# Optimization experiments

Hardware: AMD Instinct MI355X
Metric: run time of the kernel (lower is better)

Reference implementation:

```python
import jax, jax.numpy as jnp
import numpy as np

DIM = 2048
N_HEADS = 16
HEAD_DIM = DIM // N_HEADS
SEQ = 1024
BSZ = 2
ADAPTER_LEN = 10
MAX_FEATS = 10
ROPE_THETA = 10000.0


def setup_inputs() -> dict:
    key = jax.random.key(0)
    ks = jax.random.split(key, 10)
    x = jax.random.normal(ks[0], (BSZ, SEQ, DIM), dtype=jnp.float32)
    adapter = jax.random.normal(ks[1], (1, ADAPTER_LEN, DIM), dtype=jnp.float32)
    # causal additive mask [1,1,S,S]
    neg = jnp.full((SEQ, SEQ), -1e9, dtype=jnp.float32)
    mask = jnp.triu(neg, k=1)[None, None]
    # rotary frequencies (real/imag of freqs_cis)
    inv_freq = 1.0 / (ROPE_THETA ** (np.arange(0, HEAD_DIM, 2, dtype=np.float32) / HEAD_DIM))
    t = np.arange(SEQ, dtype=np.float32)
    ang = jnp.asarray(np.outer(t, inv_freq), dtype=jnp.float32)  # [S, HEAD_DIM//2]
    freqs_cos = jnp.cos(ang)
    freqs_sin = jnp.sin(ang)
    scale = 0.02
    wq = jax.random.normal(ks[2], (DIM, DIM), dtype=jnp.float32) * scale
    wk = jax.random.normal(ks[3], (DIM, DIM), dtype=jnp.float32) * scale
    wv = jax.random.normal(ks[4], (DIM, DIM), dtype=jnp.float32) * scale
    wo = jax.random.normal(ks[5], (DIM, DIM), dtype=jnp.float32) * scale
    gate1 = jax.random.normal(ks[6], (1, N_HEADS, 1, 1), dtype=jnp.float32) * 0.5
    gate2 = jnp.ones((1, N_HEADS, 1, 1), dtype=jnp.float32) * -3.0
    return {"x": x, "adapter": adapter, "mask": mask, "freqs_cos": freqs_cos,
            "freqs_sin": freqs_sin, "wq": wq, "wk": wk, "wv": wv, "wo": wo,
            "gate1": gate1, "gate2": gate2, "video_start": 30}


def _apply_rope(t, cos, sin):
    # t: [B,S,H,D]; cos/sin: [S, D//2] -> complex multiply on consecutive pairs
    tr = t.reshape(*t.shape[:-1], HEAD_DIM // 2, 2)
    xr, xi = tr[..., 0], tr[..., 1]
    c = cos[None, :, None, :]
    s = sin[None, :, None, :]
    out_r = xr * c - xi * s
    out_i = xr * s + xi * c
    return jnp.stack([out_r, out_i], axis=-1).reshape(t.shape)


def reference(x, adapter, mask, freqs_cos, freqs_sin, wq, wk, wv, wo, gate1, gate2, video_start):
    bsz, seqlen, _ = x.shape
    al = adapter.shape[1]
    vs = int(video_start)
    # projections (torch Linear: y = x @ W^T)
    xq = (x @ wq.T).reshape(bsz, seqlen, N_HEADS, HEAD_DIM)
    xk = (x @ wk.T).reshape(bsz, seqlen, N_HEADS, HEAD_DIM)
    xv = (x @ wv.T).reshape(bsz, seqlen, N_HEADS, HEAD_DIM)
    xq = _apply_rope(xq, freqs_cos, freqs_sin)
    xk = _apply_rope(xk, freqs_cos, freqs_sin)
    # adapter keys/values (no RoPE), broadcast over batch
    a_k = (adapter @ wk.T).reshape(1, al, N_HEADS, HEAD_DIM)
    a_v = (adapter @ wv.T).reshape(1, al, N_HEADS, HEAD_DIM)
    a_k = jnp.broadcast_to(a_k, (bsz, al, N_HEADS, HEAD_DIM))
    a_v = jnp.broadcast_to(a_v, (bsz, al, N_HEADS, HEAD_DIM))
    keys = jnp.concatenate([a_k, xk], axis=1)      # [B, al+S, H, D]
    values = jnp.concatenate([a_v, xv], axis=1)
    # mask extended with zeros over adapter columns
    extra = jnp.zeros((1, 1, seqlen, al), dtype=mask.dtype)
    full_mask = jnp.concatenate([extra, mask], axis=-1)
    scores = jnp.einsum('bqhd,bkhd->bhqk', xq, keys) / jnp.sqrt(jnp.float32(HEAD_DIM))
    scores = scores + full_mask
    # split softmax: adapter part gated by tanh(gate1)
    adapter_scores = jax.nn.softmax(scores[..., :al], axis=-1) * jnp.tanh(gate1)
    vt = scores[..., al:]
    vt = vt.at[:, :, vs + MAX_FEATS:, vs:vs + MAX_FEATS].add(gate2)
    vt = jax.nn.softmax(vt, axis=-1)
    probs = jnp.concatenate([adapter_scores, vt], axis=-1)  # [B,H,S,al+S]
    out = jnp.einsum('bhqk,bkhd->bqhd', probs, values)
    out = out.reshape(bsz, seqlen, DIM)
    return out @ wo.T
```

## Files before the change

### kernel.cpp

```cpp
#include <hip/hip_runtime.h>
#include <math.h>

#define DIM   2048
#define NH    16
#define HD    128
#define SEQQ  1024
#define BSZ   2
#define AL    10
#define MAXF  10
#define KVROWS (SEQQ + AL)
#define BK    32
#define VTP   2080

typedef unsigned short ushort_t;
typedef __bf16   bf16x8 __attribute__((ext_vector_type(8)));
typedef float    f32x4  __attribute__((ext_vector_type(4)));
typedef ushort_t us8    __attribute__((ext_vector_type(8)));

#define AS1 __attribute__((address_space(1)))
#define AS3 __attribute__((address_space(3)))

__device__ __forceinline__ float b2f(ushort_t u) {
    return __uint_as_float(((unsigned int)u) << 16);
}
__device__ __forceinline__ ushort_t f2b(float f) {
    unsigned int u = __float_as_uint(f);
    u += 0x7fffu + ((u >> 16) & 1u);
    return (ushort_t)(u >> 16);
}
__device__ __forceinline__ float scrub(float v, float canary) {
    return ((__float_as_uint(v) & 0x7f800000u) == 0x7f800000u) ? canary : v;
}
__device__ __forceinline__ bf16x8 cvt8(const float* p) {
    float4 a = *(const float4*)p;
    float4 b = *(const float4*)(p + 4);
    us8 u;
    u[0] = f2b(a.x); u[1] = f2b(a.y); u[2] = f2b(a.z); u[3] = f2b(a.w);
    u[4] = f2b(b.x); u[5] = f2b(b.y); u[6] = f2b(b.z); u[7] = f2b(b.w);
    return *(bf16x8*)&u;
}

__global__ __launch_bounds__(256) void cvt5(
    const float* __restrict__ s0, const float* __restrict__ s1,
    const float* __restrict__ s2, const float* __restrict__ s3,
    const float* __restrict__ s4,
    ushort_t* __restrict__ d0, ushort_t* __restrict__ d1,
    ushort_t* __restrict__ d2, ushort_t* __restrict__ d3,
    ushort_t* __restrict__ d4)
{
    const int y = blockIdx.y;
    const float* s = (y == 0) ? s0 : (y == 1) ? s1 : (y == 2) ? s2 : (y == 3) ? s3 : s4;
    ushort_t*    d = (y == 0) ? d0 : (y == 1) ? d1 : (y == 2) ? d2 : (y == 3) ? d3 : d4;
    size_t i = (size_t)blockIdx.x * 256 + threadIdx.x;
    float4 a = ((const float4*)s)[2 * i];
    float4 b = ((const float4*)s)[2 * i + 1];
    us8 u;
    u[0] = f2b(a.x); u[1] = f2b(a.y); u[2] = f2b(a.z); u[3] = f2b(a.w);
    u[4] = f2b(b.x); u[5] = f2b(b.y); u[6] = f2b(b.z); u[7] = f2b(b.w);
    *(us8*)(d + i * 8) = u;
}

__global__ __launch_bounds__(256) void adapter_gemm(
    const float* __restrict__ adp,
    const ushort_t* __restrict__ Wkb, const ushort_t* __restrict__ Wvb,
    ushort_t* __restrict__ Ko, ushort_t* __restrict__ VtO,
    float canary)
{
    __shared__ ushort_t Al[AL * DIM];

    const int t = threadIdx.x;
    #pragma unroll
    for (int p = 0; p < 10; ++p) {
        int i = p * 256 + t;
        const float* sp = adp + i * 8;
        float4 a = *(const float4*)sp;
        float4 b = *(const float4*)(sp + 4);
        us8 u;
        u[0] = f2b(a.x); u[1] = f2b(a.y); u[2] = f2b(a.z); u[3] = f2b(a.w);
        u[4] = f2b(b.x); u[5] = f2b(b.y); u[6] = f2b(b.z); u[7] = f2b(b.w);
        *(us8*)(Al + i * 8) = u;
    }
    __syncthreads();

    const int z = blockIdx.x >> 8;
    const ushort_t* W = z ? Wvb : Wkb;
    const int nbase = (blockIdx.x & 255) * 8;
    const int w = t >> 6, lane = t & 63;

    #pragma unroll
    for (int nn = 0; nn < 2; ++nn) {
        const int n = nbase + w * 2 + nn;
        const ushort_t* wr = W + (size_t)n * DIM;
        float acc[AL] = {};
        #pragma unroll
        for (int c = 0; c < 4; ++c) {
            const int k = c * 512 + lane * 8;
            us8 b8 = *(const us8*)(wr + k);
            float bf[8];
            #pragma unroll
            for (int j = 0; j < 8; ++j) bf[j] = b2f(b8[j]);
            #pragma unroll
            for (int m = 0; m < AL; ++m) {
                us8 a8 = *(const us8*)(Al + m * DIM + k);
                #pragma unroll
                for (int j = 0; j < 8; ++j)
                    acc[m] = fmaf(b2f(a8[j]), bf[j], acc[m]);
            }
        }
        #pragma unroll
        for (int m = 0; m < AL; ++m) {
            float v = acc[m];
            v += __shfl_xor(v, 1);  v += __shfl_xor(v, 2);
            v += __shfl_xor(v, 4);  v += __shfl_xor(v, 8);
            v += __shfl_xor(v, 16); v += __shfl_xor(v, 32);
            if (lane == 0) {
                ushort_t ov = f2b(scrub(v, canary));
                if (z) VtO[(size_t)n * VTP + 2048 + m] = ov;
                else   Ko[(size_t)m * DIM + n] = ov;
            }
        }
        if (z && lane < 22) VtO[(size_t)n * VTP + 2058 + lane] = 0;
    }
}

template<int MODE>
__global__ __launch_bounds__(256) void gemm_bt(
    const ushort_t* __restrict__ A,
    const ushort_t* __restrict__ B0, const ushort_t* __restrict__ B1, const ushort_t* __restrict__ B2,
    void* __restrict__ C0, void* __restrict__ C1, void* __restrict__ C2,
    const float* __restrict__ fc, const float* __restrict__ fs,
    float qscale, float canary)
{
    __shared__ ushort_t As[128 * 32];
    __shared__ ushort_t Bs[128 * 32];

    const int lid  = blockIdx.x + (blockIdx.y << 4) + (blockIdx.z << 8);
    const int cpx  = (int)(gridDim.z << 5);
    const int wgid = (lid & 7) * cpx + (lid >> 3);
    const int z    = wgid >> 8;
    const int rem  = wgid & 255;
    const int m0   = (rem >> 4) << 7;
    const int n0   = (rem & 15) << 7;

    const ushort_t* B = (z == 0) ? B0 : (z == 1) ? B1 : B2;
    void*           C = (z == 0) ? C0 : (z == 1) ? C1 : C2;

    const int t = threadIdx.x;
    const int w = t >> 6, lane = t & 63;
    const int ln = lane & 15, qd = lane >> 4;
    const int wrow = (w >> 1) * 64, wcol = (w & 1) * 64;

    const int r0 = t >> 2, c0 = (t & 3) * 8;
    const int r1 = (t + 256) >> 2;
    const ushort_t* Ag0 = A + (size_t)(m0 + r0) * DIM + c0;
    const ushort_t* Ag1 = A + (size_t)(m0 + r1) * DIM + c0;
    const ushort_t* Bg0 = B + (size_t)(n0 + r0) * DIM + c0;
    const ushort_t* Bg1 = B + (size_t)(n0 + r1) * DIM + c0;
    ushort_t* Al0 = As + (size_t)t * 8;
    ushort_t* Al1 = As + (size_t)(t + 256) * 8;
    ushort_t* Bl0 = Bs + (size_t)t * 8;
    ushort_t* Bl1 = Bs + (size_t)(t + 256) * 8;

    f32x4 acc[4][4] = {};

    for (int k0 = 0; k0 < DIM; k0 += BK) {
        if (k0) __syncthreads();
        __builtin_amdgcn_global_load_lds((const AS1 void*)(Ag0 + k0), (AS3 void*)Al0, 16, 0, 0);
        __builtin_amdgcn_global_load_lds((const AS1 void*)(Ag1 + k0), (AS3 void*)Al1, 16, 0, 0);
        __builtin_amdgcn_global_load_lds((const AS1 void*)(Bg0 + k0), (AS3 void*)Bl0, 16, 0, 0);
        __builtin_amdgcn_global_load_lds((const AS1 void*)(Bg1 + k0), (AS3 void*)Bl1, 16, 0, 0);
        __syncthreads();

        bf16x8 af[4], bfr[4];
        #pragma unroll
        for (int i = 0; i < 4; ++i) {
            af[i]  = *(const bf16x8*)(As + (wrow + i * 16 + ln) * 32 + qd * 8);
            bfr[i] = *(const bf16x8*)(Bs + (wcol + i * 16 + ln) * 32 + qd * 8);
        }
        #pragma unroll
        for (int i = 0; i < 4; ++i)
            #pragma unroll
            for (int j = 0; j < 4; ++j)
                acc[i][j] = __builtin_amdgcn_mfma_f32_16x16x32_bf16(af[i], bfr[j], acc[i][j], 0, 0, 0);
    }

    const float rsc = (MODE == 0 && z == 0) ? qscale : 1.0f;

    #pragma unroll
    for (int i = 0; i < 4; ++i) {
        #pragma unroll
        for (int j = 0; j < 4; ++j) {
            const int gn = n0 + wcol + j * 16 + ln;
            const int gm0 = m0 + wrow + i * 16 + qd * 4;
            if (MODE == 0 && z == 2) {
                ushort4 ov;
                ov.x = f2b(scrub(acc[i][j][0], canary));
                ov.y = f2b(scrub(acc[i][j][1], canary));
                ov.z = f2b(scrub(acc[i][j][2], canary));
                ov.w = f2b(scrub(acc[i][j][3], canary));
                *(ushort4*)((ushort_t*)C + (size_t)gn * VTP + gm0) = ov;
            } else if (MODE == 0) {
                const int fidx = (gn & 127) >> 1;
                #pragma unroll
                for (int r = 0; r < 4; ++r) {
                    const int gm = gm0 + r;
                    float v = scrub(acc[i][j][r], canary);
                    float po = __shfl_xor(v, 1);
                    const int fo = ((gm & 1023) << 6) + fidx;
                    float c = fc[fo], s = fs[fo];
                    float ov = (ln & 1) ? (po * s + v * c) : (v * c - po * s);
                    ((ushort_t*)C)[(size_t)gm * DIM + gn] = f2b(ov * rsc);
                }
            } else {
                #pragma unroll
                for (int r = 0; r < 4; ++r) {
                    float v = scrub(acc[i][j][r], canary);
                    ((float*)C)[(size_t)(gm0 + r) * DIM + gn] = v;
                }
            }
        }
    }
}

__global__ __launch_bounds__(256) void gemm_wo(
    const ushort_t* __restrict__ A,
    const ushort_t* __restrict__ W,
    float* __restrict__ C, float canary)
{
    __shared__ ushort_t As[128 * 32];
    __shared__ ushort_t Bs[64 * 32];

    const int lid  = blockIdx.x + (blockIdx.y << 5);
    const int wgid = (lid & 7) * 64 + (lid >> 3);
    const int m0 = (wgid >> 5) << 7;
    const int n0 = (wgid & 31) << 6;

    const int t = threadIdx.x;
    const int w = t >> 6, lane = t & 63;
    const int ln = lane & 15, qd = lane >> 4;
    const int wrow = (w >> 1) * 64, wcol = (w & 1) * 32;

    const int r0 = t >> 2, c0 = (t & 3) * 8;
    const int r1 = (t + 256) >> 2;
    const ushort_t* Ag0 = A + (size_t)(m0 + r0) * DIM + c0;
    const ushort_t* Ag1 = A + (size_t)(m0 + r1) * DIM + c0;
    const ushort_t* Bg0 = W + (size_t)(n0 + r0) * DIM + c0;
    ushort_t* Al0 = As + (size_t)t * 8;
    ushort_t* Al1 = As + (size_t)(t + 256) * 8;
    ushort_t* Bl0 = Bs + (size_t)t * 8;

    f32x4 acc[4][2] = {};

    for (int k0 = 0; k0 < DIM; k0 += BK) {
        if (k0) __syncthreads();
        __builtin_amdgcn_global_load_lds((const AS1 void*)(Ag0 + k0), (AS3 void*)Al0, 16, 0, 0);
        __builtin_amdgcn_global_load_lds((const AS1 void*)(Ag1 + k0), (AS3 void*)Al1, 16, 0, 0);
        __builtin_amdgcn_global_load_lds((const AS1 void*)(Bg0 + k0), (AS3 void*)Bl0, 16, 0, 0);
        __syncthreads();

        bf16x8 af[4], bfr[2];
        #pragma unroll
        for (int i = 0; i < 4; ++i)
            af[i] = *(const bf16x8*)(As + (wrow + i * 16 + ln) * 32 + qd * 8);
        #pragma unroll
        for (int j = 0; j < 2; ++j)
            bfr[j] = *(const bf16x8*)(Bs + (wcol + j * 16 + ln) * 32 + qd * 8);
        #pragma unroll
        for (int i = 0; i < 4; ++i)
            #pragma unroll
            for (int j = 0; j < 2; ++j)
                acc[i][j] = __builtin_amdgcn_mfma_f32_16x16x32_bf16(af[i], bfr[j], acc[i][j], 0, 0, 0);
    }

    #pragma unroll
    for (int i = 0; i < 4; ++i)
        #pragma unroll
        for (int j = 0; j < 2; ++j) {
            const int gn = n0 + wcol + j * 16 + ln;
            const int gm0 = m0 + wrow + i * 16 + qd * 4;
            #pragma unroll
            for (int r = 0; r < 4; ++r)
                C[(size_t)(gm0 + r) * DIM + gn] = scrub(acc[i][j][r], canary);
        }
}

template<bool AF32, bool CF32>
__global__ __launch_bounds__(256) void mfma_gemm(
    const void* __restrict__ Av,
    const float* __restrict__ B0, const float* __restrict__ B1, const float* __restrict__ B2,
    void* __restrict__ C0, void* __restrict__ C1, void* __restrict__ C2,
    int M, float canary)
{
    const int z = blockIdx.z;
    const float* B = (z == 0) ? B0 : (z == 1) ? B1 : B2;
    void*       C = (z == 0) ? C0 : (z == 1) ? C1 : C2;

    const int m0 = blockIdx.y * 128;
    const int n0 = blockIdx.x * 128;
    const int t    = threadIdx.x;
    const int w    = t >> 6;
    const int lane = t & 63;
    const int ln   = lane & 15, qd = lane >> 4;
    const int wrow = (w >> 1) * 64, wcol = (w & 1) * 64;

    size_t aoff[4];
    const float* brow[4];
    #pragma unroll
    for (int i = 0; i < 4; ++i) {
        int gr = m0 + wrow + i * 16 + ln; gr = (gr < M) ? gr : (M - 1);
        aoff[i] = (size_t)gr * DIM + qd * 8;
        brow[i] = B + (size_t)(n0 + wcol + i * 16 + ln) * DIM + qd * 8;
    }

    f32x4 acc[4][4] = {};

    for (int k0 = 0; k0 < DIM; k0 += BK) {
        bf16x8 af[4], bfr[4];
        #pragma unroll
        for (int i = 0; i < 4; ++i) {
            if (AF32) af[i] = cvt8((const float*)Av + aoff[i] + k0);
            else      af[i] = *(const bf16x8*)((const ushort_t*)Av + aoff[i] + k0);
            bfr[i] = cvt8(brow[i] + k0);
        }
        #pragma unroll
        for (int i = 0; i < 4; ++i)
            #pragma unroll
            for (int j = 0; j < 4; ++j)
                acc[i][j] = __builtin_amdgcn_mfma_f32_16x16x32_bf16(af[i], bfr[j], acc[i][j], 0, 0, 0);
    }

    #pragma unroll
    for (int i = 0; i < 4; ++i) {
        #pragma unroll
        for (int j = 0; j < 4; ++j) {
            const int gn = n0 + wcol + j * 16 + ln;
            #pragma unroll
            for (int r = 0; r < 4; ++r) {
                const int gm = m0 + wrow + i * 16 + qd * 4 + r;
                float v = scrub(acc[i][j][r], canary);
                if (gm < M) {
                    if (CF32) ((float*)C)[(size_t)gm * DIM + gn] = v;
                    else      ((ushort_t*)C)[(size_t)gm * DIM + gn] = f2b(v);
                }
            }
        }
    }
}

__global__ __launch_bounds__(256) void rope_kernel(ushort_t* __restrict__ Qb,
                                                   ushort_t* __restrict__ Kb,
                                                   const float* __restrict__ fc,
                                                   const float* __restrict__ fs,
                                                   float qscale)
{
    int i = blockIdx.x * 256 + threadIdx.x;
    ushort_t* T = blockIdx.y ? Kb : Qb;
    const float sc = blockIdx.y ? 1.0f : qscale;
    int row = i >> 10;
    int p   = i & 1023;
    float c = fc[((row & 1023) << 6) + (p & 63)];
    float s = fs[((row & 1023) << 6) + (p & 63)];
    ushort_t* ptr = T + (size_t)row * DIM + p * 2;
    float xr = b2f(ptr[0]), xi = b2f(ptr[1]);
    ptr[0] = f2b((xr * c - xi * s) * sc);
    ptr[1] = f2b((xr * s + xi * c) * sc);
}

__global__ __launch_bounds__(256) void attn_mfma(const ushort_t* __restrict__ Q,
                                                 const ushort_t* __restrict__ Kg,
                                                 const ushort_t* __restrict__ Vt,
                                                 const float* __restrict__ g1,
                                                 const float* __restrict__ g2,
                                                 const int* __restrict__ vsp,
                                                 ushort_t* __restrict__ AO)
{
    __shared__ ushort_t Kls[2][64 * 128];
    __shared__ ushort_t Vls[2][128 * 64];
    __shared__ ushort_t Pl[4 * 16 * 72];

    const int blk = blockIdx.x;
    const int wg   = (blk & 7) * 64 + (blk >> 3);
    const int gidx = wg >> 4;
    const int mem  = wg & 15;
    const int qtb  = (mem & 1) ? (mem >> 1) : (15 - (mem >> 1));
    const int qt   = ((gidx >> 1) & 1) ? (15 - qtb) : qtb;
    const int h = gidx & 15;
    const int b = gidx >> 4;
    const int q0  = qt * 64;
    const int nsteps = qt + 1;
    const int t = threadIdx.x;
    const int w = t >> 6, lane = t & 63;
    const int ln = lane & 15, g = lane >> 4;
    const int hb = h * HD;
    const size_t kvb = (size_t)b << 10;
    const int vs = *vsp;
    const float g2h = g2[h];
    const float ag  = tanhf(g1[h]);
    const int gq = q0 + w * 16 + ln;

    const ushort_t* qrow = Q + (kvb + gq) * DIM + hb;
    bf16x8 qf[4];
    #pragma unroll
    for (int c = 0; c < 4; ++c) qf[c] = *(const bf16x8*)(qrow + g * 8 + 32 * c);

    auto stage = [&](int bi, int k0) {
        #pragma unroll
        for (int p = 0; p < 4; ++p) {
            int i = t + 256 * p;
            int kr = i >> 4, ks = (i & 15) ^ (kr & 7);
            __builtin_amdgcn_global_load_lds(
                (const AS1 void*)(Kg + (kvb + k0 + kr) * DIM + hb + ks * 8),
                (AS3 void*)(&Kls[bi][i * 8]), 16, 0, 0);
        }
        #pragma unroll
        for (int p = 0; p < 4; ++p) {
            int i = t + 256 * p;
            int vr = i >> 3, vsl = (i & 7) ^ (vr & 7);
            __builtin_amdgcn_global_load_lds(
                (const AS1 void*)(Vt + (size_t)(hb + vr) * VTP + kvb + k0 + vsl * 8),
                (AS3 void*)(&Vls[bi][i * 8]), 16, 0, 0);
        }
    };

    stage(0, 0);

    f32x4 oa[8] = {};
    float m_run = -1e30f, l_run = 0.f;
    ushort_t* Plw = Pl + w * (16 * 72) + ln * 72;

    for (int s = 0; s < nsteps; ++s) {
        const int k0 = s * 64;
        const int cur = s & 1;
        __syncthreads();
        if (s + 1 < nsteps) stage(cur ^ 1, k0 + 64);

        f32x4 sc[4] = {};
        __builtin_amdgcn_s_setprio(1);
        #pragma unroll
        for (int mt = 0; mt < 4; ++mt) {
            const int krow = ln + 16 * mt;
            const ushort_t* krp = &Kls[cur][krow * 128];
            #pragma unroll
            for (int c = 0; c < 4; ++c) {
                bf16x8 kf = *(const bf16x8*)(krp + ((8 * g + 32 * c) ^ ((krow & 7) << 3)));
                sc[mt] = __builtin_amdgcn_mfma_f32_16x16x32_bf16(kf, qf[c], sc[mt], 0, 0, 0);
            }
        }
        __builtin_amdgcn_s_setprio(0);

        float mloc = -3e38f;
        #pragma unroll
        for (int mt = 0; mt < 4; ++mt)
            #pragma unroll
            for (int r = 0; r < 4; ++r) {
                int gk = k0 + mt * 16 + g * 4 + r;
                float v = sc[mt][r];
                if (gk > gq) v -= 1e9f;
                if (gk >= vs && gk < vs + MAXF && gq >= vs + MAXF) v += g2h;
                sc[mt][r] = v;
                mloc = fmaxf(mloc, v);
            }
        mloc = fmaxf(mloc, __shfl_xor(mloc, 16));
        mloc = fmaxf(mloc, __shfl_xor(mloc, 32));
        const float m_new = fmaxf(m_run, mloc);
        const float alpha = __expf(m_run - m_new);
        float psum = 0.f;
        #pragma unroll
        for (int mt = 0; mt < 4; ++mt) {
            float p0 = __expf(sc[mt][0] - m_new);
            float p1 = __expf(sc[mt][1] - m_new);
            float p2 = __expf(sc[mt][2] - m_new);
            float p3 = __expf(sc[mt][3] - m_new);
            psum += (p0 + p1) + (p2 + p3);
            uint2 pw_;
            pw_.x = (unsigned)f2b(p0) | ((unsigned)f2b(p1) << 16);
            pw_.y = (unsigned)f2b(p2) | ((unsigned)f2b(p3) << 16);
            *(uint2*)(Plw + mt * 16 + g * 4) = pw_;
        }
        psum += __shfl_xor(psum, 16);
        psum += __shfl_xor(psum, 32);
        l_run = l_run * alpha + psum;
        m_run = m_new;
        #pragma unroll
        for (int i = 0; i < 8; ++i) {
            oa[i][0] *= alpha; oa[i][1] *= alpha; oa[i][2] *= alpha; oa[i][3] *= alpha;
        }

        bf16x8 pf0 = *(const bf16x8*)(Plw + 8 * g);
        bf16x8 pf1 = *(const bf16x8*)(Plw + 32 + 8 * g);
        __builtin_amdgcn_s_setprio(1);
        #pragma unroll
        for (int dt = 0; dt < 8; ++dt) {
            const int vrow = dt * 16 + ln;
            const ushort_t* vrp = &Vls[cur][vrow * 64];
            bf16x8 vf0 = *(const bf16x8*)(vrp + ((g     ^ (vrow & 7)) * 8));
            bf16x8 vf1 = *(const bf16x8*)(vrp + (((g+4) ^ (vrow & 7)) * 8));
            oa[dt] = __builtin_amdgcn_mfma_f32_16x16x32_bf16(vf0, pf0, oa[dt], 0, 0, 0);
            oa[dt] = __builtin_amdgcn_mfma_f32_16x16x32_bf16(vf1, pf1, oa[dt], 0, 0, 0);
        }
        __builtin_amdgcn_s_setprio(0);
    }

    const float invl = 1.f / l_run;
    #pragma unroll
    for (int i = 0; i < 8; ++i) {
        oa[i][0] *= invl; oa[i][1] *= invl; oa[i][2] *= invl; oa[i][3] *= invl;
    }

    const ushort_t* karow = Kg + (size_t)(2048 + (ln < 10 ? ln : 9)) * DIM + hb;
    f32x4 sa4 = {};
    #pragma unroll
    for (int c = 0; c < 4; ++c) {
        bf16x8 kf = *(const bf16x8*)(karow + 8 * g + 32 * c);
        sa4 = __builtin_amdgcn_mfma_f32_16x16x32_bf16(kf, qf[c], sa4, 0, 0, 0);
    }
    float am = -3e38f;
    float pa[4];
    #pragma unroll
    for (int r = 0; r < 4; ++r) {
        int kl = g * 4 + r;
        pa[r] = (kl < 10) ? sa4[r] : -1e30f;
        am = fmaxf(am, pa[r]);
    }
    am = fmaxf(am, __shfl_xor(am, 16));
    am = fmaxf(am, __shfl_xor(am, 32));
    float asum = 0.f;
    #pragma unroll
    for (int r = 0; r < 4; ++r) { pa[r] = __expf(pa[r] - am); asum += pa[r]; }
    asum += __shfl_xor(asum, 16);
    asum += __shfl_xor(asum, 32);
    const float coef = ag / asum;
    {
        uint2 pw_;
        pw_.x = (unsigned)f2b(pa[0] * coef) | ((unsigned)f2b(pa[1] * coef) << 16);
        pw_.y = (unsigned)f2b(pa[2] * coef) | ((unsigned)f2b(pa[3] * coef) << 16);
        *(uint2*)(Plw + g * 4) = pw_;
        uint2 z2; z2.x = 0; z2.y = 0;
        *(uint2*)(Plw + 16 + g * 4) = z2;
    }
    bf16x8 paf = *(const bf16x8*)(Plw + 8 * g);
    #pragma unroll
    for (int dt = 0; dt < 8; ++dt) {
        const ushort_t* varow = Vt + (size_t)(hb + dt * 16 + ln) * VTP + 2048;
        bf16x8 vfa = *(const bf16x8*)(varow + 8 * g);
        oa[dt] = __builtin_amdgcn_mfma_f32_16x16x32_bf16(vfa, paf, oa[dt], 0, 0, 0);
    }

    ushort_t* outp = AO + (kvb + gq) * DIM + hb;
    #pragma unroll
    for (int dt = 0; dt < 8; ++dt) {
        ushort4 ov;
        ov.x = f2b(scrub(oa[dt][0], 1e8f));
        ov.y = f2b(scrub(oa[dt][1], 1e8f));
        ov.z = f2b(scrub(oa[dt][2], 1e8f));
        ov.w = f2b(scrub(oa[dt][3], 1e8f));
        *(ushort4*)(outp + dt * 16 + g * 4) = ov;
    }
}

__global__ __launch_bounds__(256) void attn_kernel(const ushort_t* __restrict__ Q,
                                                   const ushort_t* __restrict__ Kg,
                                                   const ushort_t* __restrict__ Vg,
                                                   const float* __restrict__ g1,
                                                   const float* __restrict__ g2,
                                                   const int* __restrict__ vsp,
                                                   ushort_t* __restrict__ AO)
{
    __shared__ float Qs[32 * 132];
    __shared__ float Ks[32 * 132];
    __shared__ float Vs[32 * 132];
    __shared__ float Ps[32 * 32];

    const int blk = blockIdx.x;
    const int q0  = (31 - (blk & 31)) * 32;
    const int h   = blk >> 5;
    const int t   = threadIdx.x;
    const int qi  = t >> 3;
    const int l8  = t & 7;
    const int vs  = *vsp;
    const int g_q = q0 + qi;
    const float scale = 0.08838834764831845f;
    const float g2h = g2[h];
    const float ag  = tanhf(g1[h]);

    #pragma unroll
    for (int p = 0; p < 4; ++p) {
        int idx = (p * 256 + t) * 4;
        int r = idx >> 7, d = idx & 127;
        ushort4 q4 = *(const ushort4*)(Q + (size_t)(q0 + r) * DIM + h * HD + d);
        *(float4*)(Qs + r * 132 + d) = make_float4(b2f(q4.x), b2f(q4.y), b2f(q4.z), b2f(q4.w));
    }

    float o[16];
    #pragma unroll
    for (int i = 0; i < 16; ++i) o[i] = 0.f;
    float m_run = -1e30f, l_run = 0.f;

    for (int k0 = 0; k0 <= q0 + 31; k0 += 32) {
        __syncthreads();
        #pragma unroll
        for (int p = 0; p < 4; ++p) {
            int idx = (p * 256 + t) * 4;
            int r = idx >> 7, d = idx & 127;
            size_t goff = (size_t)(k0 + r) * DIM + h * HD + d;
            ushort4 k4 = *(const ushort4*)(Kg + goff);
            ushort4 v4 = *(const ushort4*)(Vg + goff);
            *(float4*)(Ks + r * 132 + d) = make_float4(b2f(k4.x), b2f(k4.y), b2f(k4.z), b2f(k4.w));
            *(float4*)(Vs + r * 132 + d) = make_float4(b2f(v4.x), b2f(v4.y), b2f(v4.z), b2f(v4.w));
        }
        __syncthreads();

        float s[4];
        #pragma unroll
        for (int jj = 0; jj < 4; ++jj) s[jj] = 0.f;
        #pragma unroll 4
        for (int d = 0; d < 128; d += 4) {
            const float4 qv = *(const float4*)(Qs + qi * 132 + d);
            #pragma unroll
            for (int jj = 0; jj < 4; ++jj) {
                const float4 kv = *(const float4*)(Ks + (l8 + 8 * jj) * 132 + d);
                s[jj] += qv.x * kv.x + qv.y * kv.y + qv.z * kv.z + qv.w * kv.w;
            }
        }
        float mloc = -1e30f;
        #pragma unroll
        for (int jj = 0; jj < 4; ++jj) {
            int gk = k0 + l8 + 8 * jj;
            float sv = s[jj] * scale;
            if (gk > g_q) sv -= 1e9f;
            if (gk >= vs && gk < vs + MAXF && g_q >= vs + MAXF) sv += g2h;
            s[jj] = sv;
            mloc = fmaxf(mloc, sv);
        }
        mloc = fmaxf(mloc, __shfl_xor(mloc, 1));
        mloc = fmaxf(mloc, __shfl_xor(mloc, 2));
        mloc = fmaxf(mloc, __shfl_xor(mloc, 4));
        const float m_new = fmaxf(m_run, mloc);
        const float alpha = expf(m_run - m_new);
        float psum = 0.f;
        #pragma unroll
        for (int jj = 0; jj < 4; ++jj) {
            float pv = expf(s[jj] - m_new);
            psum += pv;
            Ps[qi * 32 + l8 + 8 * jj] = pv;
        }
        psum += __shfl_xor(psum, 1);
        psum += __shfl_xor(psum, 2);
        psum += __shfl_xor(psum, 4);
        l_run = l_run * alpha + psum;
        m_run = m_new;
        #pragma unroll
        for (int i = 0; i < 16; ++i) o[i] *= alpha;
        __syncthreads();

        #pragma unroll 4
        for (int kk = 0; kk < 32; ++kk) {
            const float pp = Ps[qi * 32 + kk];
            const float* vr = Vs + kk * 132 + l8 * 4;
            #pragma unroll
            for (int jj = 0; jj < 4; ++jj) {
                const float4 v4 = *(const float4*)(vr + jj * 32);
                o[jj*4+0] = fmaf(pp, v4.x, o[jj*4+0]);
                o[jj*4+1] = fmaf(pp, v4.y, o[jj*4+1]);
                o[jj*4+2] = fmaf(pp, v4.z, o[jj*4+2]);
                o[jj*4+3] = fmaf(pp, v4.w, o[jj*4+3]);
            }
        }
    }

    const float invl = 1.f / l_run;
    #pragma unroll
    for (int i = 0; i < 16; ++i) o[i] *= invl;

    __syncthreads();
    #pragma unroll
    for (int p = 0; p < 2; ++p) {
        int idx = p * 256 + t;
        if (idx < 320) {
            int fi = idx * 4; int r = fi >> 7; int d = fi & 127;
            size_t goff = (size_t)(SEQQ + r) * DIM + h * HD + d;
            ushort4 k4 = *(const ushort4*)(Kg + goff);
            ushort4 v4 = *(const ushort4*)(Vg + goff);
            *(float4*)(Ks + r * 132 + d) = make_float4(b2f(k4.x), b2f(k4.y), b2f(k4.z), b2f(k4.w));
            *(float4*)(Vs + r * 132 + d) = make_float4(b2f(v4.x), b2f(v4.y), b2f(v4.z), b2f(v4.w));
        }
    }
    __syncthreads();
    float sa[2] = {-1e30f, -1e30f};
    #pragma unroll
    for (int jj = 0; jj < 2; ++jj) {
        int kk = l8 + 8 * jj;
        if (kk < AL) {
            float acc = 0.f;
            #pragma unroll 4
            for (int d = 0; d < 128; d += 4) {
                const float4 qv = *(const float4*)(Qs + qi * 132 + d);
                const float4 kv = *(const float4*)(Ks + kk * 132 + d);
                acc += qv.x * kv.x + qv.y * kv.y + qv.z * kv.z + qv.w * kv.w;
            }
            sa[jj] = acc * scale;
        }
    }
    float am = fmaxf(sa[0], sa[1]);
    am = fmaxf(am, __shfl_xor(am, 1));
    am = fmaxf(am, __shfl_xor(am, 2));
    am = fmaxf(am, __shfl_xor(am, 4));
    float pa0 = expf(sa[0] - am);
    float pa1 = (l8 < 2) ? expf(sa[1] - am) : 0.f;
    float asum = pa0 + pa1;
    asum += __shfl_xor(asum, 1);
    asum += __shfl_xor(asum, 2);
    asum += __shfl_xor(asum, 4);
    const float coef = ag / asum;
    Ps[qi * 32 + l8] = pa0 * coef;
    if (l8 < 2) Ps[qi * 32 + 8 + l8] = pa1 * coef;
    __syncthreads();
    #pragma unroll
    for (int kk = 0; kk < AL; ++kk) {
        const float pp = Ps[qi * 32 + kk];
        const float* vr = Vs + kk * 132 + l8 * 4;
        #pragma unroll
        for (int jj = 0; jj < 4; ++jj) {
            const float4 v4 = *(const float4*)(vr + jj * 32);
            o[jj*4+0] = fmaf(pp, v4.x, o[jj*4+0]);
            o[jj*4+1] = fmaf(pp, v4.y, o[jj*4+1]);
            o[jj*4+2] = fmaf(pp, v4.z, o[jj*4+2]);
            o[jj*4+3] = fmaf(pp, v4.w, o[jj*4+3]);
        }
    }

    ushort_t* outp = AO + (size_t)g_q * DIM + h * HD + l8 * 4;
    #pragma unroll
    for (int jj = 0; jj < 4; ++jj) {
        ushort4 ov;
        ov.x = f2b(scrub(o[jj*4+0], 1e8f));
        ov.y = f2b(scrub(o[jj*4+1], 1e8f));
        ov.z = f2b(scrub(o[jj*4+2], 1e8f));
        ov.w = f2b(scrub(o[jj*4+3], 1e8f));
        *(ushort4*)(outp + jj * 32) = ov;
    }
}

extern "C" void kernel_launch(void* const* d_in, const int* in_sizes, int n_in,
                              void* d_out, int out_size, void* d_ws, size_t ws_size,
                              hipStream_t stream)
{
    const float* x   = (const float*)d_in[0];
    const float* adp = (const float*)d_in[1];
    const float* fc  = (const float*)d_in[3];
    const float* fs  = (const float*)d_in[4];
    const float* wq  = (const float*)d_in[5];
    const float* wk  = (const float*)d_in[6];
    const float* wv  = (const float*)d_in[7];
    const float* wo  = (const float*)d_in[8];
    const float* g1  = (const float*)d_in[9];
    const float* g2  = (const float*)d_in[10];
    const int*   vsp = (const int*)d_in[11];

    float* out = (float*)d_out;

    const size_t rows2 = (size_t)BSZ * SEQQ;
    const size_t qe2 = rows2 * DIM;
    const size_t ke2 = (rows2 + AL) * DIM;
    const size_t vte = (size_t)DIM * VTP;
    const size_t we  = (size_t)DIM * DIM;
    const size_t xe  = (size_t)BSZ * SEQQ * DIM;
    const size_t need = (qe2 + ke2 + vte + xe + 4 * we) * sizeof(ushort_t);

    if (ws_size >= need) {
        ushort_t* Qb  = (ushort_t*)d_ws;
        ushort_t* Kb  = Qb + qe2;
        ushort_t* VtG = Kb + ke2;
        ushort_t* Xb  = VtG + vte;
        ushort_t* Wqb = Xb + xe;
        ushort_t* Wkb = Wqb + we;
        ushort_t* Wvb = Wkb + we;
        ushort_t* Wob = Wvb + we;

        cvt5<<<dim3(2048, 5), 256, 0, stream>>>(wq, wk, wv, wo, x,
                                                Wqb, Wkb, Wvb, Wob, Xb);

        adapter_gemm<<<512, 256, 0, stream>>>(adp, Wkb, Wvb,
                                              Kb + rows2 * DIM, VtG,
                                              100.0f);

        gemm_bt<0><<<dim3(16, 16, 3), 256, 0, stream>>>(
            Xb, Wqb, Wkb, Wvb, Qb, Kb, VtG,
            fc, fs, 0.08838834764831845f, 1e5f);

        attn_mfma<<<512, 256, 0, stream>>>(Qb, Kb, VtG, g1, g2, vsp, Qb );

        gemm_wo<<<dim3(32, 16), 256, 0, stream>>>(Qb, Wob, out, 1e12f);
    } else {
        const size_t qe = (size_t)SEQQ * DIM;
        const size_t ke = (size_t)KVROWS * DIM;
        ushort_t* Qb = (ushort_t*)d_ws;
        ushort_t* Kb = Qb + qe;
        ushort_t* Vb = Kb + ke;

        mfma_gemm<true, false><<<dim3(16, 1, 2), 256, 0, stream>>>(
            adp, wk, wv, wv,
            Kb + qe, Vb + qe, Vb,
            AL, 100.0f);

        for (int b = 0; b < BSZ; ++b) {
            const long xo = (long)b * SEQQ * DIM;
            mfma_gemm<true, false><<<dim3(16, 8, 3), 256, 0, stream>>>(
                x + xo, wq, wk, wv, Qb, Kb, Vb, SEQQ, 1e5f);

            rope_kernel<<<dim3(4096, 2), 256, 0, stream>>>(Qb, Kb, fc, fs, 1.0f);

            attn_kernel<<<NH * (SEQQ / 32), 256, 0, stream>>>(Qb, Kb, Vb, g1, g2, vsp, Qb);

            mfma_gemm<false, true><<<dim3(16, 8, 1), 256, 0, stream>>>(
                Qb, wo, wo, wo, out + xo, out + xo, out + xo, SEQQ, 1e12f);
        }
    }
}
```

Before: 287.5 us.

## Double GEMM K-tile to 64 with XOR-swizzled LDS layout

The projection GEMM kernel now stages 64-wide K slices per iteration instead of 32, halving the number of barrier pairs per tile. The LDS layout uses an XOR swizzle on 16-byte chunks, applied on the global-load side and undone on the fragment reads, to avoid bank conflicts on the 128-byte row stride. Launch bounds now request 4 blocks per SM. The trade-off is doubled shared memory per block and a register cap that could cause spills.

```diff
diff --git a/kernel.cpp b/kernel.cpp
--- a/kernel.cpp
+++ b/kernel.cpp
@@ -124,15 +124,15 @@
 }
 
 template<int MODE>
-__global__ __launch_bounds__(256) void gemm_bt(
+__global__ __launch_bounds__(256, 4) void gemm_bt(
     const ushort_t* __restrict__ A,
     const ushort_t* __restrict__ B0, const ushort_t* __restrict__ B1, const ushort_t* __restrict__ B2,
     void* __restrict__ C0, void* __restrict__ C1, void* __restrict__ C2,
     const float* __restrict__ fc, const float* __restrict__ fs,
     float qscale, float canary)
 {
-    __shared__ ushort_t As[128 * 32];
-    __shared__ ushort_t Bs[128 * 32];
+    __shared__ ushort_t As[128 * 64];
+    __shared__ ushort_t Bs[128 * 64];
 
     const int lid  = blockIdx.x + (blockIdx.y << 4) + (blockIdx.z << 8);
     const int cpx  = (int)(gridDim.z << 5);
@@ -150,38 +150,45 @@
     const int ln = lane & 15, qd = lane >> 4;
     const int wrow = (w >> 1) * 64, wcol = (w & 1) * 64;
 
-    const int r0 = t >> 2, c0 = (t & 3) * 8;
-    const int r1 = (t + 256) >> 2;
-    const ushort_t* Ag0 = A + (size_t)(m0 + r0) * DIM + c0;
-    const ushort_t* Ag1 = A + (size_t)(m0 + r1) * DIM + c0;
-    const ushort_t* Bg0 = B + (size_t)(n0 + r0) * DIM + c0;
-    const ushort_t* Bg1 = B + (size_t)(n0 + r1) * DIM + c0;
-    ushort_t* Al0 = As + (size_t)t * 8;
-    ushort_t* Al1 = As + (size_t)(t + 256) * 8;
-    ushort_t* Bl0 = Bs + (size_t)t * 8;
-    ushort_t* Bl1 = Bs + (size_t)(t + 256) * 8;
+    const ushort_t* Agp[4]; const ushort_t* Bgp[4];
+    ushort_t* Alp[4]; ushort_t* Blp[4];
+    #pragma unroll
+    for (int p = 0; p < 4; ++p) {
+        int i = t + 256 * p;
+        int row = i >> 3, sl = (i & 7) ^ (row & 7);
+        Agp[p] = A + (size_t)(m0 + row) * DIM + sl * 8;
+        Bgp[p] = B + (size_t)(n0 + row) * DIM + sl * 8;
+        Alp[p] = As + (size_t)i * 8;
+        Blp[p] = Bs + (size_t)i * 8;
+    }
 
     f32x4 acc[4][4] = {};
 
-    for (int k0 = 0; k0 < DIM; k0 += BK) {
+    for (int k0 = 0; k0 < DIM; k0 += 64) {
         if (k0) __syncthreads();
-        __builtin_amdgcn_global_load_lds((const AS1 void*)(Ag0 + k0), (AS3 void*)Al0, 16, 0, 0);
-        __builtin_amdgcn_global_load_lds((const AS1 void*)(Ag1 + k0), (AS3 void*)Al1, 16, 0, 0);
-        __builtin_amdgcn_global_load_lds((const AS1 void*)(Bg0 + k0), (AS3 void*)Bl0, 16, 0, 0);
-        __builtin_amdgcn_global_load_lds((const AS1 void*)(Bg1 + k0), (AS3 void*)Bl1, 16, 0, 0);
+        #pragma unroll
+        for (int p = 0; p < 4; ++p) {
+            __builtin_amdgcn_global_load_lds((const AS1 void*)(Agp[p] + k0), (AS3 void*)Alp[p], 16, 0, 0);
+            __builtin_amdgcn_global_load_lds((const AS1 void*)(Bgp[p] + k0), (AS3 void*)Blp[p], 16, 0, 0);
+        }
         __syncthreads();
 
-        bf16x8 af[4], bfr[4];
-        #pragma unroll
-        for (int i = 0; i < 4; ++i) {
-            af[i]  = *(const bf16x8*)(As + (wrow + i * 16 + ln) * 32 + qd * 8);
-            bfr[i] = *(const bf16x8*)(Bs + (wcol + i * 16 + ln) * 32 + qd * 8);
-        }
-        #pragma unroll
-        for (int i = 0; i < 4; ++i)
-            #pragma unroll
-            for (int j = 0; j < 4; ++j)
-                acc[i][j] = __builtin_amdgcn_mfma_f32_16x16x32_bf16(af[i], bfr[j], acc[i][j], 0, 0, 0);
+        #pragma unroll
+        for (int kk = 0; kk < 2; ++kk) {
+            bf16x8 af[4], bfr[4];
+            #pragma unroll
+            for (int i = 0; i < 4; ++i) {
+                const int ar = wrow + i * 16 + ln;
+                const int br = wcol + i * 16 + ln;
+                af[i]  = *(const bf16x8*)(As + (size_t)ar * 64 + (((kk << 2) + qd) ^ (ar & 7)) * 8);
+                bfr[i] = *(const bf16x8*)(Bs + (size_t)br * 64 + (((kk << 2) + qd) ^ (br & 7)) * 8);
+            }
+            #pragma unroll
+            for (int i = 0; i < 4; ++i)
+                #pragma unroll
+                for (int j = 0; j < 4; ++j)
+                    acc[i][j] = __builtin_amdgcn_mfma_f32_16x16x32_bf16(af[i], bfr[j], acc[i][j], 0, 0, 0);
+        }
     }
 
     const float rsc = (MODE == 0 && z == 0) ? qscale : 1.0f;
```

Result: slower. 294.0 us (+2.2%).
